# Optimization experiments

Measured on AMD Instinct MI355X. Metric: run time of the kernel, lower is better.

The kernel has to match this reference:

```python
import jax, jax.numpy as jnp
import numpy as np

SL, BS, HS = 2048, 4, 1024
FFN, E, TOPK = 4096, 8, 2
T = SL * BS


def setup_inputs() -> dict:
    key = jax.random.key(0)
    k1, k2, k3, k4, k5 = jax.random.split(key, 5)
    x = jax.random.normal(k1, (SL, BS, HS), dtype=jnp.float32)
    expert_weights = jax.random.uniform(k2, (T, TOPK), dtype=jnp.float32)
    w1 = jax.random.normal(k3, (E, HS, FFN), dtype=jnp.float32) * (HS ** -0.5)
    w2 = jax.random.normal(k4, (E, FFN, HS), dtype=jnp.float32) * (FFN ** -0.5)
    expert_indices = jax.random.randint(k5, (T, TOPK), 0, E, dtype=jnp.int32)
    return {"x": x, "expert_weights": expert_weights, "w1": w1, "w2": w2,
            "expert_indices": expert_indices}


def reference(x, expert_weights, w1, w2, expert_indices):
    """Dropless MoE: dispatch each token to its top_k experts, run the
    per-expert MLP (x @ W1 -> gelu -> @ W2), combine weighted copies.

    Equivalent math to megablocks sort/gather -> grouped GEMM -> scatter:
    each (token, k) row is processed by exactly expert_indices[t, k]'s MLP
    and the results are summed back per token with expert_weights.
    """
    in_shape = x.shape
    hs = x.shape[-1]
    xf = x.reshape(-1, hs)                      # [T, H]
    top_k = expert_indices.shape[-1]
    eids = expert_indices.reshape(-1)           # [T*top_k]
    # gather: replicate each token top_k times (row j <-> token j // top_k)
    x_rep = jnp.repeat(xf, top_k, axis=0)       # [T*top_k, H]

    def per_expert(acc, ewb):
        e, w1_e, w2_e = ewb
        h = jax.nn.gelu(x_rep @ w1_e)           # [T*top_k, F]
        y = h @ w2_e                            # [T*top_k, H]
        mask = (eids == e).astype(x.dtype)[:, None]
        return acc + mask * y, None

    n_exp = w1.shape[0]
    acc0 = jnp.zeros_like(x_rep)
    out_flat, _ = jax.lax.scan(per_expert, acc0, (jnp.arange(n_exp), w1, w2))
    # scatter-combine: weighted sum of the top_k expert outputs per token
    w_flat = expert_weights.reshape(-1, 1)      # [T*top_k, 1]
    out = (w_flat * out_flat).reshape(-1, top_k, hs).sum(axis=1)
    return out.reshape(in_shape)
```

## Files before the change

### kernel.cpp

```cpp
#include <hip/hip_runtime.h>
#include <hip/hip_bf16.h>
#include <stdint.h>
#include <stddef.h>

#define SLEN 2048
#define BSZ  4
#define HSD  1024
#define FFND 4096
#define NEXP 8
#define NTOP 2
#define NTOK (SLEN*BSZ)
#define NROW (NTOK*NTOP)
#define NRP  (NROW + NEXP*256)
#define MAXT (NROW/256 + NEXP)

typedef __hip_bfloat16 bf16;
typedef __attribute__((ext_vector_type(8))) __bf16 b8v;
typedef __attribute__((ext_vector_type(4))) float f4v;

static constexpr size_t OFF_BLOCKHIST = 0;
static constexpr size_t OFF_BLOCKBASE = 2048;
static constexpr size_t OFF_SCHED_E   = 4096;
static constexpr size_t OFF_SCHED_R   = 4736;
static constexpr size_t OFF_NTILES    = 5376;
static constexpr size_t OFF_STOK      = 8192;
static constexpr size_t OFF_SWT       = OFF_STOK + 73728;
static constexpr size_t OFF_SLOT      = OFF_SWT + 73728;
static constexpr size_t OFF_XB        = 221184;
static constexpr size_t OFF_W1T       = OFF_XB  + (size_t)NTOK*HSD*2;
static constexpr size_t OFF_W2T       = OFF_W1T + (size_t)NEXP*FFND*HSD*2;
static constexpr size_t OFF_H         = OFF_W2T + (size_t)NEXP*HSD*FFND*2;
static constexpr size_t WS_NEED       = OFF_H   + (size_t)NRP*FFND*2;
static constexpr size_t OFF_YP        = OFF_XB;

__device__ __forceinline__ void gload_lds16(const void* g, void* l) {
  __builtin_amdgcn_global_load_lds(
      (const __attribute__((address_space(1))) unsigned int*)g,
      (__attribute__((address_space(3))) unsigned int*)l, 16, 0, 0);
}

__device__ __forceinline__ f4v mfma16(b8v a, b8v b, f4v c) {
  return __builtin_amdgcn_mfma_f32_16x16x32_bf16(a, b, c, 0, 0, 0);
}

__device__ __forceinline__ float gelu_tanh(float x) {
  float u = 0.7978845608028654f * x * (1.0f + 0.044715f * x * x);
  float e = __expf(2.0f * u);
  float t = 1.0f - 2.0f / (e + 1.0f);
  return 0.5f * x * (1.0f + t);
}

#define NB_CONV (NTOK*HSD/4/256)
#define NB_W1   (NEXP*(HSD/64)*(FFND/32))
#define NB_W2   (NEXP*(FFND/64)*(HSD/32))
#define NB_HIST 64
#define NB_PREP (NB_CONV + NB_W1 + NB_W2 + NB_HIST)

template<int R, int C>
__device__ __forceinline__ void transpose_body(const float* __restrict__ src,
                                               bf16* __restrict__ dst,
                                               int l, int tid) {
  __shared__ float tile[32][65];
  constexpr int CT = C / 32, RT = R / 64;
  int e   = l / (CT * RT);
  int rem = l - e * (CT * RT);
  int by  = rem / CT, bx = rem % CT;
  const float* s = src + (size_t)e * R * C;
  uint* d = (uint*)((ushort*)dst + (size_t)e * R * C);
  int c0 = bx * 32, r0 = by * 64;
  int tx = tid & 31, ty = tid >> 5;
  #pragma unroll
  for (int j = 0; j < 64; j += 8)
    tile[tx][ty + j] = s[(size_t)(r0 + ty + j) * C + (c0 + tx)];
  __syncthreads();
  #pragma unroll
  for (int j = 0; j < 32; j += 8) {
    int c = ty + j;
    alignas(4) bf16 p[2];
    p[0] = __float2bfloat16(tile[c][tx * 2]);
    p[1] = __float2bfloat16(tile[c][tx * 2 + 1]);
    d[(((size_t)(c0 + c) * R + r0) >> 1) + tx] = *(const uint*)p;
  }
}

__global__ void moe_prep(const float* __restrict__ x, bf16* __restrict__ xb,
                         const float* __restrict__ w1, bf16* __restrict__ w1t,
                         const float* __restrict__ w2, bf16* __restrict__ w2t,
                         const int* __restrict__ eidx, int* __restrict__ blockhist) {
  int bid = blockIdx.x;
  int tid = threadIdx.x;
  if (bid < NB_CONV) {
    int gid = bid * 256 + tid;
    float4 v = ((const float4*)x)[gid];
    alignas(8) bf16 o[4];
    o[0] = __float2bfloat16(v.x); o[1] = __float2bfloat16(v.y);
    o[2] = __float2bfloat16(v.z); o[3] = __float2bfloat16(v.w);
    ((ushort4*)xb)[gid] = *(const ushort4*)o;
  } else if (bid < NB_CONV + NB_W1) {
    transpose_body<HSD, FFND>(w1, w1t, bid - NB_CONV, tid);
  } else if (bid < NB_CONV + NB_W1 + NB_W2) {
    transpose_body<FFND, HSD>(w2, w2t, bid - NB_CONV - NB_W1, tid);
  } else {
    __shared__ int h[NEXP];
    int b = bid - NB_CONV - NB_W1 - NB_W2;
    if (tid < NEXP) h[tid] = 0;
    __syncthreads();
    int gid = b * 256 + tid;
    atomicAdd(&h[eidx[gid] & 7], 1);
    __syncthreads();
    if (tid < NEXP) blockhist[b * NEXP + tid] = h[tid];
  }
}

__global__ void moe_plan(const int* __restrict__ blockhist, int* __restrict__ blockbase,
                         int* __restrict__ sched_e, int* __restrict__ sched_r,
                         int* __restrict__ ntiles,
                         int* __restrict__ stok, float* __restrict__ swt) {
  __shared__ int h[64 * NEXP];
  __shared__ int cnt[NEXP], off[NEXP];
  int tid = threadIdx.x;
  for (int i = tid; i < NRP; i += 256) { stok[i] = 0; swt[i] = 0.0f; }
  for (int i = tid; i < 64 * NEXP; i += 256) h[i] = blockhist[i];
  __syncthreads();
  if (tid < NEXP) {
    int c = 0;
    #pragma unroll
    for (int b = 0; b < 64; ++b) c += h[b * NEXP + tid];
    cnt[tid] = c;
  }
  __syncthreads();
  if (tid == 0) {
    int run = 0, it = 0;
    for (int e = 0; e < NEXP; ++e) {
      off[e] = run;
      int nt = (cnt[e] + 255) >> 8;
      for (int j = 0; j < nt; ++j) { sched_e[it] = e; sched_r[it] = run + j * 256; ++it; }
      run += nt << 8;
    }
    *ntiles = it;
  }
  __syncthreads();
  if (tid < NEXP) {
    int r = off[tid];
    #pragma unroll
    for (int b = 0; b < 64; ++b) { blockbase[b * NEXP + tid] = r; r += h[b * NEXP + tid]; }
  }
}

__global__ void moe_scatter(const int* __restrict__ eidx, const float* __restrict__ ew,
                            const int* __restrict__ blockbase,
                            int* __restrict__ stok, float* __restrict__ swt,
                            int* __restrict__ slot) {
  __shared__ int cur[NEXP];
  int tid = threadIdx.x;
  if (tid < NEXP) cur[tid] = blockbase[blockIdx.x * NEXP + tid];
  __syncthreads();
  int gid = blockIdx.x * 256 + tid;
  int e = eidx[gid] & 7;
  int pos = atomicAdd(&cur[e], 1);
  stok[pos] = gid >> 1;
  swt[pos]  = ew[gid];
  slot[gid] = pos;
}

template<int KDIM, int NDIM, int NSPLIT, bool GATHER, int ACT, int GX, int NWG>
__global__ __launch_bounds__(512, 2)
void moe_gemm(const bf16* __restrict__ A, const bf16* __restrict__ B,
              bf16* __restrict__ OutBase,
              const int* __restrict__ stok,
              const int* __restrict__ sched_e, const int* __restrict__ sched_r,
              const int* __restrict__ ntiles) {
  constexpr int BM = 256, BN = 256, BK = 64;
  constexpr int BUFS = (BM + BN) * BK;
  constexpr int KT = KDIM / BK / NSPLIT;
  constexpr int JT = KT / 2;
  static_assert(NWG % 8 == 0, "XCD swizzle needs nwg % 8 == 0");
  constexpr unsigned Q = NWG / 8;

  unsigned flat = (blockIdx.z * MAXT + blockIdx.y) * GX + blockIdx.x;
  unsigned nf = (flat & 7) * Q + (flat >> 3);
  const int bx = nf % GX;
  unsigned t2 = nf / GX;
  const int rt = t2 % MAXT;
  const int z  = t2 / MAXT;

  if (rt >= *ntiles) return;
  const int tid  = threadIdx.x;
  const int lane = tid & 63;
  const int wid  = tid >> 6;
  const int wm = wid & 1, wn = wid >> 1;
  const int e    = sched_e[rt];
  const int row0 = sched_r[rt];
  const int n0   = bx * BN;
  const int kbase = z * (KDIM / NSPLIT);
  bf16* Out = OutBase + (size_t)z * NRP * NDIM;

  __shared__ short lds[2 * BUFS];

  const int l15  = lane & 15;
  const int quad = lane >> 4;
  const int xor7 = l15 & 7;
  const ushort* Aus  = (const ushort*)A;
  const ushort* Bexp = (const ushort*)B + (size_t)e * NDIM * KDIM;

  const int rsub  = lane >> 3;
  const int kgsrc = (lane & 7) ^ rsub;
  const ushort* aP[2][2];
  const ushort* bP[2][2];
  #pragma unroll
  for (int h = 0; h < 2; ++h)
    #pragma unroll
    for (int q = 0; q < 2; ++q) {
      int xr = 128 * h + 8 * (2 * wid + q) + rsub;
      int grow = GATHER ? stok[row0 + xr] : (row0 + xr);
      aP[h][q] = Aus  + (size_t)grow * KDIM + kbase + kgsrc * 8;
      bP[h][q] = Bexp + (size_t)(n0 + xr) * KDIM + kbase + kgsrc * 8;
    }

  auto SA = [&](int b, int h, int T) {
    #pragma unroll
    for (int q = 0; q < 2; ++q)
      gload_lds16(aP[h][q] + T * 64, lds + b * BUFS + h * 8192 + (2 * wid + q) * 512);
  };
  auto SB = [&](int b, int h, int T) {
    #pragma unroll
    for (int q = 0; q < 2; ++q)
      gload_lds16(bP[h][q] + T * 64, lds + b * BUFS + BM * BK + h * 8192 + (2 * wid + q) * 512);
  };

  const int goff0 = (quad ^ xor7) << 3;
  const int goff1 = ((4 + quad) ^ xor7) << 3;
  const int mbase = (wm * 128 + l15) * 64;
  const int nbase = BM * BK + (wn * 64 + l15) * 64;

  f4v acc[8][4];
  #pragma unroll
  for (int mt = 0; mt < 8; ++mt)
    #pragma unroll
    for (int nt = 0; nt < 4; ++nt) acc[mt][nt] = (f4v)0.0f;

  b8v aF[2][4], bF0[2][2], bF1[2][2];

  auto LDA = [&](int b, int qm) {
    const short* base = lds + b * BUFS + mbase + qm * 4096;
    #pragma unroll
    for (int t = 0; t < 4; ++t) {
      aF[0][t] = *(const b8v*)(base + t * 1024 + goff0);
      aF[1][t] = *(const b8v*)(base + t * 1024 + goff1);
    }
  };
  auto LDB = [&](int b, int qn, b8v (&bF)[2][2]) {
    const short* base = lds + b * BUFS + nbase + qn * 2048;
    #pragma unroll
    for (int u = 0; u < 2; ++u) {
      bF[0][u] = *(const b8v*)(base + u * 1024 + goff0);
      bF[1][u] = *(const b8v*)(base + u * 1024 + goff1);
    }
  };
  auto MM = [&](int qm, int qn, b8v (&bF)[2][2]) {
    __builtin_amdgcn_s_setprio(1);
    #pragma unroll
    for (int s = 0; s < 2; ++s)
      #pragma unroll
      for (int t = 0; t < 4; ++t)
        #pragma unroll
        for (int u = 0; u < 2; ++u)
          acc[qm * 4 + t][qn * 2 + u] = mfma16(aF[s][t], bF[s][u], acc[qm * 4 + t][qn * 2 + u]);
    __builtin_amdgcn_s_setprio(0);
  };
  auto BAR = [&] {
    asm volatile("" ::: "memory");
    __builtin_amdgcn_s_barrier();
    asm volatile("" ::: "memory");
  };

  SB(0, 0, 0); SB(0, 1, 0); SA(0, 0, 0); SA(0, 1, 0);
  SB(1, 0, 1); SB(1, 1, 1);
  asm volatile("s_waitcnt vmcnt(4)" ::: "memory");
  __builtin_amdgcn_s_barrier();
  asm volatile("" ::: "memory");

  #pragma unroll 1
  for (int j = 0; j < JT; ++j) {
    const int t1 = 2 * j + 1, t2i = 2 * j + 2, t3 = 2 * j + 3;
    const bool more = (j + 1 < JT);
    LDA(0, 0); LDB(0, 0, bF0);
    SA(1, 0, t1);
    BAR(); MM(0, 0, bF0); BAR();
    LDB(0, 1, bF1);
    SA(1, 1, t1);
    BAR(); MM(0, 1, bF1); BAR();
    LDA(0, 1);
    if (more) SB(0, 0, t2i);
    BAR(); MM(1, 1, bF1); BAR();
    if (more) SB(0, 1, t2i);
    BAR(); MM(1, 0, bF0);
    if (more) asm volatile("s_waitcnt vmcnt(4)" ::: "memory");
    else      asm volatile("s_waitcnt vmcnt(0)" ::: "memory");
    BAR();
    LDA(1, 0); LDB(1, 0, bF0);
    if (more) SA(0, 0, t2i);
    BAR(); MM(0, 0, bF0); BAR();
    LDB(1, 1, bF1);
    if (more) SA(0, 1, t2i);
    BAR(); MM(0, 1, bF1); BAR();
    LDA(1, 1);
    if (more) SB(1, 0, t3);
    BAR(); MM(1, 1, bF1); BAR();
    if (more) SB(1, 1, t3);
    BAR(); MM(1, 0, bF0);
    asm volatile("s_waitcnt vmcnt(4)" ::: "memory");
    BAR();
  }

  #pragma unroll
  for (int mt = 0; mt < 8; ++mt)
    #pragma unroll
    for (int nt = 0; nt < 4; ++nt) {
      f4v v = acc[mt][nt];
      #pragma unroll
      for (int r = 0; r < 4; ++r) {
        int m = row0 + wm * 128 + mt * 16 + quad * 4 + r;
        int n = n0   + wn * 64  + nt * 16 + l15;
        float o = (ACT == 0) ? gelu_tanh(v[r]) : v[r];
        Out[(size_t)m * NDIM + n] = __float2bfloat16(o);
      }
    }
}

__global__ void moe_combine(const bf16* __restrict__ Yp, const float* __restrict__ swt,
                            const int* __restrict__ slot, float* __restrict__ out) {
  int gid = blockIdx.x * 256 + threadIdx.x;
  int t  = gid >> 7;
  int ho = (gid & 127) << 3;
  int s0 = slot[t * 2], s1 = slot[t * 2 + 1];
  float w0 = swt[s0], w1 = swt[s1];
  const __bf16* Y0 = (const __bf16*)Yp;
  const __bf16* Y1 = Y0 + (size_t)NRP * HSD;
  b8v a0 = *(const b8v*)(Y0 + (size_t)s0 * HSD + ho);
  b8v a1 = *(const b8v*)(Y1 + (size_t)s0 * HSD + ho);
  b8v b0 = *(const b8v*)(Y0 + (size_t)s1 * HSD + ho);
  b8v b1 = *(const b8v*)(Y1 + (size_t)s1 * HSD + ho);
  float o[8];
  #pragma unroll
  for (int i = 0; i < 8; ++i)
    o[i] = w0 * ((float)a0[i] + (float)a1[i]) + w1 * ((float)b0[i] + (float)b1[i]);
  float4* op = (float4*)(out + (size_t)t * HSD + ho);
  op[0] = make_float4(o[0], o[1], o[2], o[3]);
  op[1] = make_float4(o[4], o[5], o[6], o[7]);
}

extern "C" void kernel_launch(void* const* d_in, const int* in_sizes, int n_in,
                              void* d_out, int out_size, void* d_ws, size_t ws_size,
                              hipStream_t stream) {
  const float* x    = (const float*)d_in[0];
  const float* ew   = (const float*)d_in[1];
  const float* w1   = (const float*)d_in[2];
  const float* w2   = (const float*)d_in[3];
  const int*   eidx = (const int*)d_in[4];
  float* out = (float*)d_out;
  char* ws = (char*)d_ws;

  if (ws_size < WS_NEED) {
    hipMemsetAsync(d_out, 0x7F, 8, stream);
    return;
  }

  int*   blockhist = (int*)(ws + OFF_BLOCKHIST);
  int*   blockbase = (int*)(ws + OFF_BLOCKBASE);
  int*   sched_e   = (int*)(ws + OFF_SCHED_E);
  int*   sched_r   = (int*)(ws + OFF_SCHED_R);
  int*   ntiles    = (int*)(ws + OFF_NTILES);
  int*   stok      = (int*)(ws + OFF_STOK);
  float* swt       = (float*)(ws + OFF_SWT);
  int*   slot      = (int*)(ws + OFF_SLOT);
  bf16*  xb        = (bf16*)(ws + OFF_XB);
  bf16*  w1t       = (bf16*)(ws + OFF_W1T);
  bf16*  w2t       = (bf16*)(ws + OFF_W2T);
  bf16*  Hbuf      = (bf16*)(ws + OFF_H);
  bf16*  Ypart     = (bf16*)(ws + OFF_YP);

  moe_prep<<<NB_PREP, 256, 0, stream>>>(x, xb, w1, w1t, w2, w2t, eidx, blockhist);
  moe_plan<<<1, 256, 0, stream>>>(blockhist, blockbase, sched_e, sched_r, ntiles, stok, swt);
  moe_scatter<<<64, 256, 0, stream>>>(eidx, ew, blockbase, stok, swt, slot);

  moe_gemm<HSD, FFND, 1, true, 0, FFND/256, (FFND/256)*MAXT>
      <<<dim3(FFND / 256, MAXT, 1), 512, 0, stream>>>(
      xb, w1t, Hbuf, stok, sched_e, sched_r, ntiles);
  moe_gemm<FFND, HSD, 2, false, 1, HSD/256, (HSD/256)*MAXT*2>
      <<<dim3(HSD / 256, MAXT, 2), 512, 0, stream>>>(
      Hbuf, w2t, Ypart, stok, sched_e, sched_r, ntiles);

  moe_combine<<<NTOK * HSD / 8 / 256, 256, 0, stream>>>(Ypart, swt, slot, out);
}
```

Baseline: 701.7 us.

## Stage GEMM epilogue through LDS for vector stores, simplify GELU, drop XCD swizzle

The GEMM epilogue now writes activated tiles into a per-wave LDS slab and then stores 16-byte vectors per row, instead of scattered 2-byte global stores. GELU is rewritten in the equivalent sigmoid form with fewer operations. The XCD-aware block index remapping is removed in favour of direct blockIdx mapping. That could reduce L2 locality across chiplets.

```diff
diff --git a/kernel.cpp b/kernel.cpp
--- a/kernel.cpp
+++ b/kernel.cpp
@@ -43,11 +43,9 @@
   return __builtin_amdgcn_mfma_f32_16x16x32_bf16(a, b, c, 0, 0, 0);
 }
 
-__device__ __forceinline__ float gelu_tanh(float x) {
-  float u = 0.7978845608028654f * x * (1.0f + 0.044715f * x * x);
-  float e = __expf(2.0f * u);
-  float t = 1.0f - 2.0f / (e + 1.0f);
-  return 0.5f * x * (1.0f + t);
+__device__ __forceinline__ float gelu_fast(float x) {
+  float u2 = x * (1.5957691216057308f + 0.07135481627286064f * x * x);
+  return x / (1.0f + __expf(-u2));
 }
 
 #define NB_CONV (NTOK*HSD/4/256)
@@ -163,7 +161,7 @@
   slot[gid] = pos;
 }
 
-template<int KDIM, int NDIM, int NSPLIT, bool GATHER, int ACT, int GX, int NWG>
+template<int KDIM, int NDIM, int NSPLIT, bool GATHER, int ACT>
 __global__ __launch_bounds__(512, 2)
 void moe_gemm(const bf16* __restrict__ A, const bf16* __restrict__ B,
               bf16* __restrict__ OutBase,
@@ -174,16 +172,8 @@
   constexpr int BUFS = (BM + BN) * BK;
   constexpr int KT = KDIM / BK / NSPLIT;
   constexpr int JT = KT / 2;
-  static_assert(NWG % 8 == 0, "XCD swizzle needs nwg % 8 == 0");
-  constexpr unsigned Q = NWG / 8;
-
-  unsigned flat = (blockIdx.z * MAXT + blockIdx.y) * GX + blockIdx.x;
-  unsigned nf = (flat & 7) * Q + (flat >> 3);
-  const int bx = nf % GX;
-  unsigned t2 = nf / GX;
-  const int rt = t2 % MAXT;
-  const int z  = t2 / MAXT;
-
+
+  int rt = blockIdx.y;
   if (rt >= *ntiles) return;
   const int tid  = threadIdx.x;
   const int lane = tid & 63;
@@ -191,7 +181,8 @@
   const int wm = wid & 1, wn = wid >> 1;
   const int e    = sched_e[rt];
   const int row0 = sched_r[rt];
-  const int n0   = bx * BN;
+  const int n0   = blockIdx.x * BN;
+  const int z    = blockIdx.z;
   const int kbase = z * (KDIM / NSPLIT);
   bf16* Out = OutBase + (size_t)z * NRP * NDIM;
 
@@ -313,19 +304,34 @@
     BAR();
   }
 
-  #pragma unroll
-  for (int mt = 0; mt < 8; ++mt)
-    #pragma unroll
-    for (int nt = 0; nt < 4; ++nt) {
-      f4v v = acc[mt][nt];
+  {
+    constexpr int SST = 72;
+    bf16* slab = (bf16*)(lds + wid * 4608);
+    const int r8 = lane >> 3;
+    const int c8 = (lane & 7) * 8;
+    ushort* outb = (ushort*)Out;
+    #pragma unroll
+    for (int mh = 0; mh < 2; ++mh) {
       #pragma unroll
-      for (int r = 0; r < 4; ++r) {
-        int m = row0 + wm * 128 + mt * 16 + quad * 4 + r;
-        int n = n0   + wn * 64  + nt * 16 + l15;
-        float o = (ACT == 0) ? gelu_tanh(v[r]) : v[r];
-        Out[(size_t)m * NDIM + n] = __float2bfloat16(o);
+      for (int mt = 0; mt < 4; ++mt)
+        #pragma unroll
+        for (int nt = 0; nt < 4; ++nt) {
+          f4v v = acc[mh * 4 + mt][nt];
+          #pragma unroll
+          for (int r = 0; r < 4; ++r) {
+            float o = (ACT == 0) ? gelu_fast(v[r]) : v[r];
+            slab[(mt * 16 + quad * 4 + r) * SST + nt * 16 + l15] = __float2bfloat16(o);
+          }
+        }
+      #pragma unroll
+      for (int i = 0; i < 8; ++i) {
+        int r = i * 8 + r8;
+        b8v vv = *(const b8v*)((const short*)slab + r * SST + c8);
+        *(b8v*)(outb + (size_t)(row0 + wm * 128 + mh * 64 + r) * NDIM
+                      + (n0 + wn * 64 + c8)) = vv;
       }
     }
+  }
 }
 
 __global__ void moe_combine(const bf16* __restrict__ Yp, const float* __restrict__ swt,
@@ -384,11 +390,9 @@
   moe_plan<<<1, 256, 0, stream>>>(blockhist, blockbase, sched_e, sched_r, ntiles, stok, swt);
   moe_scatter<<<64, 256, 0, stream>>>(eidx, ew, blockbase, stok, swt, slot);
 
-  moe_gemm<HSD, FFND, 1, true, 0, FFND/256, (FFND/256)*MAXT>
-      <<<dim3(FFND / 256, MAXT, 1), 512, 0, stream>>>(
+  moe_gemm<HSD, FFND, 1, true, 0><<<dim3(FFND / 256, MAXT, 1), 512, 0, stream>>>(
       xb, w1t, Hbuf, stok, sched_e, sched_r, ntiles);
-  moe_gemm<FFND, HSD, 2, false, 1, HSD/256, (HSD/256)*MAXT*2>
-      <<<dim3(HSD / 256, MAXT, 2), 512, 0, stream>>>(
+  moe_gemm<FFND, HSD, 2, false, 1><<<dim3(HSD / 256, MAXT, 2), 512, 0, stream>>>(
       Hbuf, w2t, Ypart, stok, sched_e, sched_r, ntiles);
 
   moe_combine<<<NTOK * HSD / 8 / 256, 256, 0, stream>>>(Ypart, swt, slot, out);
```

New measurement: 697.4 us. No clear change (-0.6%).
